# Kernel tuning notes

Measured on AMD Instinct MI355X. Metric: run time of the kernel, lower is better.

The kernel has to match this reference:

```python
import math
import jax, jax.numpy as jnp
import numpy as np

MAX_CH = 21
D_CONV = 1024
LAT_DIM = 5
N_HEADS = 2            # TST_encoder hard-codes n_heads=2 (not PatchTSTEncoder's n_heads=8)
D_FF = 256
L_RAW = 38400
CONV_SPECS = [(512, 10, 5, 1), (512, 3, 2, 1), (512, 3, 2, 1), (1024, 3, 2, 1)]  # (dim,k,stride,dilation)
T_FRAMES = 959         # ((((38400-10)//5+1 -3)//2+1 -3)//2+1 -3)//2+1
T_TOTAL = MAX_CH * T_FRAMES  # 20139
L_LAT = MAX_CH * LAT_DIM     # 105


def sinusoid_table(n, d):
    pos = jnp.arange(n, dtype=jnp.float32)[:, None]
    div = jnp.exp(jnp.arange(0, d, 2, dtype=jnp.float32) * (-math.log(10000.0) / d))
    pe = jnp.zeros((n, d), jnp.float32)
    pe = pe.at[:, 0::2].set(jnp.sin(pos * div))
    pe = pe.at[:, 1::2].set(jnp.cos(pos * div))
    return pe


def setup_inputs() -> dict:
    key = jax.random.key(0)
    ks = jax.random.split(key, 16)
    x = jax.random.normal(ks[0], (1, MAX_CH, L_RAW), dtype=jnp.float32)
    # per-channel validity mask: first 17 of 21 channels valid, broadcast over frames
    ch_valid = jnp.arange(MAX_CH) < 17
    ch_mask = jnp.repeat(ch_valid, T_FRAMES)[None, None, :]  # (1,1,T_TOTAL) bool

    conv_params = {}
    in_c = 1
    for i, (dim, k, s, dil) in enumerate(CONV_SPECS):
        std = 1.0 / math.sqrt(in_c * k)
        conv_params[f"conv_w{i+1}"] = jax.random.normal(ks[1 + i], (dim, in_c, k), jnp.float32) * std
        conv_params[f"conv_b{i+1}"] = jnp.zeros((dim,), jnp.float32)
        in_c = dim

    ch_emb = sinusoid_table(MAX_CH, D_CONV)  # trainable channel embedding, sinusoidal init
    latent_q = jax.random.normal(ks[6], (L_LAT, D_CONV), jnp.float32) * math.sqrt(2.0 / (L_LAT + D_CONV))
    std_d = 1.0 / math.sqrt(D_CONV)
    wk_w = jax.random.normal(ks[7], (D_CONV, D_CONV), jnp.float32) * std_d
    wk_b = jnp.zeros((D_CONV,), jnp.float32)
    wv_w = jax.random.normal(ks[8], (D_CONV, D_CONV), jnp.float32) * std_d
    wv_b = jnp.zeros((D_CONV,), jnp.float32)
    ff_w1 = jax.random.normal(ks[9], (D_FF, D_CONV), jnp.float32) * std_d   # Linear(d_conv->d_ff), no bias
    ff_w2 = jax.random.normal(ks[10], (D_CONV, D_FF), jnp.float32) * (1.0 / math.sqrt(D_FF))
    return dict(x=x,
                conv_w1=conv_params["conv_w1"], conv_b1=conv_params["conv_b1"],
                conv_w2=conv_params["conv_w2"], conv_b2=conv_params["conv_b2"],
                conv_w3=conv_params["conv_w3"], conv_b3=conv_params["conv_b3"],
                conv_w4=conv_params["conv_w4"], conv_b4=conv_params["conv_b4"],
                ch_emb=ch_emb, latent_q=latent_q,
                wk_w=wk_w, wk_b=wk_b, wv_w=wv_w, wv_b=wv_b,
                ff_w1=ff_w1, ff_w2=ff_w2, ch_mask=ch_mask)


def _conv1d(x, w, b, stride, dilation):
    # x: (N, C_in, L), w: (C_out, C_in, K)
    y = jax.lax.conv_general_dilated(x, w, window_strides=(stride,), padding='VALID',
                                     rhs_dilation=(dilation,),
                                     dimension_numbers=('NCH', 'OIH', 'NCH'))
    return y + b[None, :, None]


def reference(x, conv_w1, conv_b1, conv_w2, conv_b2, conv_w3, conv_b3, conv_w4, conv_b4,
              ch_emb, latent_q, wk_w, wk_b, wv_w, wv_b, ff_w1, ff_w2, ch_mask):
    b, c_in, L = x.shape
    # --- ConvFeatureExtraction: per-channel conv stack (dropout is identity at eval) ---
    h = x.reshape(b * c_in, 1, L)
    weights = [(conv_w1, conv_b1), (conv_w2, conv_b2), (conv_w3, conv_b3), (conv_w4, conv_b4)]
    for (w, bi), (_, k, s, dil) in zip(weights, CONV_SPECS):
        h = jax.nn.gelu(_conv1d(h, w, bi, s, dil), approximate=False)
    t = h.shape[-1]
    x_conv = h.reshape(b, c_in, D_CONV, t).transpose(0, 1, 3, 2)  # (b, c_in, t, d_conv)

    # --- DataEmbedding: temporal sinusoid (buffer) + channel embedding (param) ---
    pe = sinusoid_table(t, D_CONV)                                # (t, d_conv)
    x_pos = x_conv + pe[None, None] + ch_emb[None, :, None, :]
    u = x_pos.reshape(b, c_in * t, D_CONV)                        # (1, T, d_conv)

    # --- perceiver_resampler (pre_norm=False: no LayerNorms applied) ---
    T = u.shape[1]
    d_h = D_CONV // N_HEADS
    lq = latent_q.reshape(1, N_HEADS, L_LAT, d_h)                 # exact torch .view semantics
    kproj = (u @ wk_w.T + wk_b).reshape(b, T, N_HEADS, d_h)
    vproj = (u @ wv_w.T + wv_b).reshape(b, T, N_HEADS, d_h)
    k = kproj.transpose(0, 2, 3, 1)                               # (b, H, d, T)
    v = vproj.transpose(0, 2, 1, 3)                               # (b, H, T, d)
    scale = N_HEADS ** (-0.5)                                     # note: heads, not d_k
    scores = jnp.einsum('bhld,bhdt->bhlt', lq, k) * scale         # (b, H, L_lat, T)
    mask = ch_mask[:, None, :, :]                                 # (b,1,1,T) -> broadcast
    scores = jnp.where(mask, scores, -1000000000.0)
    attn = jax.nn.softmax(scores, axis=-1)
    attn = jnp.where(mask, attn, 0.0)
    o = jnp.einsum('bhlt,bhtd->bhld', attn, v)                    # (b, H, L_lat, d)
    o = o.transpose(0, 2, 1, 3).reshape(b, L_LAT, D_CONV)

    # --- GELU FFN (bias=False) + residual ---
    ffn = jax.nn.gelu(o @ ff_w1.T, approximate=False) @ ff_w2.T
    return o + ffn
```

## Files before the change

kernel.cpp:

```cpp
#include <hip/hip_runtime.h>
#include <math.h>


#define NCH 17
#define LRAW 38400
#define LC1 7679
#define LC2 3839
#define LC3 1919
#define LC4 959
#define XA1 3840
#define XA2 1920
#define XA3 960
#define DC 1024
#define TVALID (NCH * LC4)
#define TPAD 16320
#define LLAT 105
#define DH 512
#define ASTR 40
#define GMAX 9
#define ESTR 132

typedef unsigned short u16;
typedef __attribute__((ext_vector_type(8))) short bf16x8;
typedef __attribute__((ext_vector_type(4))) float f32x4;

__device__ __forceinline__ float bf2f(u16 s) {
    union { unsigned int u; float f; } cv; cv.u = ((unsigned int)s) << 16; return cv.f;
}
__device__ __forceinline__ u16 f2bf(float f) {
    union { float f; unsigned int u; } cv; cv.f = f;
    unsigned int u = cv.u;
    u += 0x7FFFu + ((u >> 16) & 1u);
    return (u16)(u >> 16);
}
__device__ __forceinline__ float gelu_exact(float x) {
    return 0.5f * x * (1.0f + erff(x * 0.70710678118654752f));
}
__device__ __forceinline__ float gelu_fast(float x) {
    float u = 0.7978845608f * x * (1.0f + 0.044715f * x * x);
    u = fminf(fmaxf(u, -9.0f), 9.0f);
    float e = __expf(2.0f * u);
    return 0.5f * x * (1.0f + (e - 1.0f) / (e + 1.0f));
}

__device__ __forceinline__ void gload16(const u16* g, u16* l) {
    __builtin_amdgcn_global_load_lds(
        (const __attribute__((address_space(1))) void*)g,
        (__attribute__((address_space(3))) void*)l, 16, 0, 0);
}

__device__ __forceinline__ int xcd_logical(int d, int N) {
    int q = N >> 3, r = N & 7, x = d & 7, j = d >> 3;
    return (x < r ? x * (q + 1) : r * (q + 1) + (x - r) * q) + j;
}

#define STAGE_TILE(lds, src, row0, ld, k0)                                          \
    {                                                                               \
        int m_ = tid >> 2, c_ = tid & 3;                                            \
        gload16(&(src)[(size_t)((row0) + m_) * (ld) + (k0) + ((c_ ^ ((m_ >> 1) & 3)) << 3)], \
                &(lds)[m_ * 32 + c_ * 8]);                                          \
        int m2_ = m_ + 64;                                                          \
        gload16(&(src)[(size_t)((row0) + m2_) * (ld) + (k0) + ((c_ ^ ((m2_ >> 1) & 3)) << 3)], \
                &(lds)[m2_ * 32 + c_ * 8]);                                         \
    }

#define FRAG(lds, R) \
    (*reinterpret_cast<const bf16x8*>(&(lds)[(R) * 32 + ((l4 ^ (((R) >> 1) & 3)) << 3)]))

__global__ void __launch_bounds__(256) cvt_kernel(
        const float* __restrict__ in, u16* __restrict__ out, int n) {
    int i = blockIdx.x * 256 + threadIdx.x;
    if (i < n) out[i] = f2bf(in[i]);
}

__global__ void __launch_bounds__(256) wsplit_kernel(
        const float* __restrict__ w, u16* __restrict__ out, int dout) {
    int idx = blockIdx.x * 256 + threadIdx.x;
    if (idx >= dout * 1536) return;
    int d = idx / 1536, k = idx - d * 1536;
    int ci = k / 3, jj = k - ci * 3;
    out[((size_t)jj * dout + d) * 512 + ci] = f2bf(w[idx]);
}

__global__ void __launch_bounds__(256) lqcvt_kernel(
        const float* __restrict__ lq, u16* __restrict__ lqbf) {
    int idx = blockIdx.x * 256 + threadIdx.x;
    if (idx >= 2 * 128 * 512) return;
    int h = idx >> 16, rem = idx & 65535;
    int m = rem >> 9, k = rem & 511;
    lqbf[idx] = (m < LLAT) ? f2bf(lq[(size_t)h * LLAT * DH + m * DH + k]) : (u16)0;
}

__global__ void __launch_bounds__(256) pe_kernel(float* __restrict__ pe) {
    int idx = blockIdx.x * 256 + threadIdx.x;
    if (idx >= LC4 * 512) return;
    int t = idx / 512, i = idx - (idx / 512) * 512;
    float f = expf((-2.0f * (float)i) * (9.210340371976184f / 1024.0f));
    float ang = (float)t * f;
    pe[t * DC + 2 * i]     = sinf(ang);
    pe[t * DC + 2 * i + 1] = cosf(ang);
}

__global__ void __launch_bounds__(256) conv1_kernel(
        const float* __restrict__ x, const float* __restrict__ w1,
        const float* __restrict__ b1, u16* __restrict__ out, int g0) {
    __shared__ float xs[64 * 5 + 5];
    int cg = blockIdx.y;
    int c  = g0 + cg;
    int t0 = blockIdx.x * 64;
    int nseg = min(64, LC1 - t0);
    int xlen = nseg * 5 + 5;
    const float* xrow = x + (size_t)c * LRAW + t0 * 5;
    int tid = threadIdx.x;
    if (tid < xlen) xs[tid] = xrow[tid];
    if (tid + 256 < xlen) xs[tid + 256] = xrow[tid + 256];
    int d0 = tid * 2;
    float wr0[10], wr1[10];
    #pragma unroll
    for (int j = 0; j < 10; ++j) {
        wr0[j] = w1[d0 * 10 + j];
        wr1[j] = w1[(d0 + 1) * 10 + j];
    }
    float bb0 = b1[d0], bb1 = b1[d0 + 1];
    __syncthreads();
    u16* outc = out + (size_t)cg * 2 * XA1 * 512;
    for (int tt = 0; tt < nseg; ++tt) {
        float a0 = bb0, a1 = bb1;
        #pragma unroll
        for (int j = 0; j < 10; ++j) {
            float xv = xs[tt * 5 + j];
            a0 += wr0[j] * xv;
            a1 += wr1[j] * xv;
        }
        int t = t0 + tt;
        ushort2 wv;
        wv.x = f2bf(gelu_fast(a0));
        wv.y = f2bf(gelu_fast(a1));
        *reinterpret_cast<ushort2*>(
            &outc[((size_t)(t & 1) * XA1 + (t >> 1)) * 512 + d0]) = wv;
    }
}

template <int DOUT, int XIN, int XOUT, int LOUT, int EPI, int NNT, int NMT>
__global__ void __launch_bounds__(256, 4) conv_mfma(
        const u16* __restrict__ in, const u16* __restrict__ wsplit,
        const float* __restrict__ bias, u16* __restrict__ out,
        const float* __restrict__ pe, const float* __restrict__ chemb,
        int g0) {
    __shared__ __align__(16) u16 SH[128 * ESTR];
    u16* const Asb[2] = {SH, SH + 4096};
    u16* const Bsb[2] = {SH + 8192, SH + 12288};
    int L = xcd_logical(blockIdx.x, gridDim.x);
    int mt = L % NMT;
    int rest = L / NMT;
    int nt = rest % NNT;
    int cg = rest / NNT;
    int m0 = mt * 128, n0 = nt * 128;
    int tid = threadIdx.x, lane = tid & 63, wave = tid >> 6;
    int wm = (wave >> 1) * 64, wn = (wave & 1) * 64;
    int l15 = lane & 15, l4 = lane >> 4;
    const u16* bufc = in + (size_t)cg * 2 * XIN * 512;
    const u16* wjp[3] = {wsplit, wsplit + (size_t)DOUT * 512,
                         wsplit + 2 * (size_t)DOUT * 512};
    const u16* bjp[3] = {bufc, bufc + (size_t)XIN * 512, bufc + 512};
    f32x4 acc[4][4] = {};

#define C_STAGE(s, buf)                                   \
    {                                                     \
        int jj_ = (s) >> 4, kk_ = ((s) & 15) << 5;        \
        STAGE_TILE(Asb[buf], wjp[jj_], m0, 512, kk_);     \
        STAGE_TILE(Bsb[buf], bjp[jj_], n0, 512, kk_);     \
    }
#define C_COMPUTE(buf)                                                        \
    {                                                                         \
        bf16x8 af[4], bfr[4];                                                 \
        _Pragma("unroll")                                                     \
        for (int mi = 0; mi < 4; ++mi) af[mi]  = FRAG(Asb[buf], wm + mi * 16 + l15); \
        _Pragma("unroll")                                                     \
        for (int ni = 0; ni < 4; ++ni) bfr[ni] = FRAG(Bsb[buf], wn + ni * 16 + l15); \
        _Pragma("unroll")                                                     \
        for (int mi = 0; mi < 4; ++mi)                                        \
            _Pragma("unroll")                                                 \
            for (int ni = 0; ni < 4; ++ni)                                    \
                acc[mi][ni] = __builtin_amdgcn_mfma_f32_16x16x32_bf16(        \
                    af[mi], bfr[ni], acc[mi][ni], 0, 0, 0);                   \
    }

    C_STAGE(0, 0);
    __syncthreads();
    for (int s = 0; s < 48; s += 2) {
        C_STAGE(s + 1, 1);
        C_COMPUTE(0);
        __syncthreads();
        if (s + 2 < 48) C_STAGE(s + 2, 0);
        C_COMPUTE(1);
        __syncthreads();
    }
#undef C_STAGE
#undef C_COMPUTE

    #pragma unroll
    for (int mi = 0; mi < 4; ++mi) {
        int ml = wm + mi * 16 + l4 * 4;
        #pragma unroll
        for (int ni = 0; ni < 4; ++ni) {
            int nl = wn + ni * 16 + l15;
            ushort4 sv;
            sv.x = f2bf(acc[mi][ni][0]); sv.y = f2bf(acc[mi][ni][1]);
            sv.z = f2bf(acc[mi][ni][2]); sv.w = f2bf(acc[mi][ni][3]);
            *reinterpret_cast<ushort4*>(&SH[nl * ESTR + ml]) = sv;
        }
    }
    __syncthreads();
    int row = tid >> 1, half = tid & 1;
    int t = n0 + row;
    if (t < LOUT) {
        const u16* srow = &SH[row * ESTR + half * 64];
        int d0 = m0 + half * 64;
        if (EPI == 0) {
            u16* dst = out + ((size_t)cg * 2 + (t & 1)) * (size_t)XOUT * 512
                           + (size_t)(t >> 1) * 512 + d0;
            #pragma unroll
            for (int q = 0; q < 8; ++q) {
                bf16x8 sv = *reinterpret_cast<const bf16x8*>(&srow[q * 8]);
                bf16x8 ov;
                #pragma unroll
                for (int e = 0; e < 8; ++e)
                    ov[e] = (short)f2bf(gelu_fast(bf2f((u16)sv[e]) + bias[d0 + q * 8 + e]));
                *reinterpret_cast<bf16x8*>(&dst[q * 8]) = ov;
            }
        } else {
            int c = g0 + cg;
            u16* dst = out + ((size_t)c * LC4 + t) * DC + d0;
            const float* per = &pe[(size_t)t * DC + d0];
            const float* chr = &chemb[(size_t)c * DC + d0];
            #pragma unroll
            for (int q = 0; q < 8; ++q) {
                bf16x8 sv = *reinterpret_cast<const bf16x8*>(&srow[q * 8]);
                bf16x8 ov;
                #pragma unroll
                for (int e = 0; e < 8; ++e)
                    ov[e] = (short)f2bf(gelu_fast(bf2f((u16)sv[e]) + bias[d0 + q * 8 + e])
                                        + per[q * 8 + e] + chr[q * 8 + e]);
                *reinterpret_cast<bf16x8*>(&dst[q * 8]) = ov;
            }
        }
    }
}

__global__ void __launch_bounds__(256, 4) projkv_mfma(
        const u16* __restrict__ u, const u16* __restrict__ wkv,
        const float* __restrict__ kb, const float* __restrict__ vb,
        u16* __restrict__ K, u16* __restrict__ Vt) {
    __shared__ __align__(16) u16 SH[128 * ESTR];
    u16* const Asb[2] = {SH, SH + 4096};
    u16* const Bsb[2] = {SH + 8192, SH + 12288};
    int L = xcd_logical(blockIdx.x, gridDim.x);
    int nt = L & 15;
    int mt = L >> 4;
    int m0 = mt * 128, n0 = nt * 128;
    int tid = threadIdx.x, lane = tid & 63, wave = tid >> 6;
    int wm = (wave >> 1) * 64, wn = (wave & 1) * 64;
    int l15 = lane & 15, l4 = lane >> 4;
    f32x4 acc[4][4] = {};

#define P_STAGE(s, buf)                               \
    {                                                 \
        int kk_ = (s) << 5;                           \
        STAGE_TILE(Asb[buf], u,   m0, DC, kk_);       \
        STAGE_TILE(Bsb[buf], wkv, n0, DC, kk_);       \
    }
#define P_COMPUTE(buf)                                                        \
    {                                                                         \
        bf16x8 af[4], bfr[4];                                                 \
        _Pragma("unroll")                                                     \
        for (int mi = 0; mi < 4; ++mi) af[mi]  = FRAG(Asb[buf], wm + mi * 16 + l15); \
        _Pragma("unroll")                                                     \
        for (int ni = 0; ni < 4; ++ni) bfr[ni] = FRAG(Bsb[buf], wn + ni * 16 + l15); \
        _Pragma("unroll")                                                     \
        for (int mi = 0; mi < 4; ++mi)                                        \
            _Pragma("unroll")                                                 \
            for (int ni = 0; ni < 4; ++ni)                                    \
                acc[mi][ni] = __builtin_amdgcn_mfma_f32_16x16x32_bf16(        \
                    af[mi], bfr[ni], acc[mi][ni], 0, 0, 0);                   \
    }

    P_STAGE(0, 0);
    __syncthreads();
    for (int s = 0; s < 32; s += 2) {
        P_STAGE(s + 1, 1);
        P_COMPUTE(0);
        __syncthreads();
        if (s + 2 < 32) P_STAGE(s + 2, 0);
        P_COMPUTE(1);
        __syncthreads();
    }
#undef P_STAGE
#undef P_COMPUTE

    if (n0 < 1024) {
        #pragma unroll
        for (int mi = 0; mi < 4; ++mi) {
            int ml = wm + mi * 16 + l4 * 4;
            #pragma unroll
            for (int ni = 0; ni < 4; ++ni) {
                int nl = wn + ni * 16 + l15;
                #pragma unroll
                for (int r = 0; r < 4; ++r)
                    SH[(ml + r) * ESTR + nl] = f2bf(acc[mi][ni][r]);
            }
        }
        __syncthreads();
        int row = tid >> 1, half = tid & 1;
        int t = m0 + row;
        if (t < TVALID) {
            const u16* srow = &SH[row * ESTR + half * 64];
            int nn = n0 + half * 64;
            u16* dst = K + (size_t)t * DC + nn;
            #pragma unroll
            for (int q = 0; q < 8; ++q) {
                bf16x8 sv = *reinterpret_cast<const bf16x8*>(&srow[q * 8]);
                bf16x8 ov;
                #pragma unroll
                for (int e = 0; e < 8; ++e)
                    ov[e] = (short)f2bf(bf2f((u16)sv[e]) + kb[nn + q * 8 + e]);
                *reinterpret_cast<bf16x8*>(&dst[q * 8]) = ov;
            }
        }
    } else {
        #pragma unroll
        for (int mi = 0; mi < 4; ++mi) {
            int ml = wm + mi * 16 + l4 * 4;
            #pragma unroll
            for (int ni = 0; ni < 4; ++ni) {
                int nl = wn + ni * 16 + l15;
                ushort4 sv;
                sv.x = f2bf(acc[mi][ni][0]); sv.y = f2bf(acc[mi][ni][1]);
                sv.z = f2bf(acc[mi][ni][2]); sv.w = f2bf(acc[mi][ni][3]);
                *reinterpret_cast<ushort4*>(&SH[nl * ESTR + ml]) = sv;
            }
        }
        __syncthreads();
        int row = tid >> 1, half = tid & 1;
        int j = (n0 - 1024) + row;
        int tbase = m0 + half * 64;
        if (tbase < TPAD) {
            float bj = vb[j];
            const u16* srow = &SH[row * ESTR + half * 64];
            u16* dst = Vt + (size_t)j * TPAD + tbase;
            #pragma unroll
            for (int q = 0; q < 8; ++q) {
                bf16x8 sv = *reinterpret_cast<const bf16x8*>(&srow[q * 8]);
                bf16x8 ov;
                #pragma unroll
                for (int e = 0; e < 8; ++e)
                    ov[e] = (short)f2bf(bf2f((u16)sv[e]) + bj);
                *reinterpret_cast<bf16x8*>(&dst[q * 8]) = ov;
            }
        }
    }
}

__global__ void __launch_bounds__(256) scores_mfma(
        const u16* __restrict__ lqbf, const u16* __restrict__ K,
        float* __restrict__ sc) {
    __shared__ __align__(16) u16 As[128 * ASTR];
    __shared__ __align__(16) u16 Bs[128 * ASTR];
    int n0 = blockIdx.x * 128;
    int h  = blockIdx.y;
    int tid = threadIdx.x, lane = tid & 63, wave = tid >> 6;
    int wm = (wave >> 1) * 64, wn = (wave & 1) * 64;
    int l15 = lane & 15, l4 = lane >> 4;
    const u16* lqh = lqbf + (size_t)h * 128 * DH;
    f32x4 acc[4][4] = {};
    for (int k0 = 0; k0 < DH; k0 += 32) {
        #pragma unroll
        for (int p = 0; p < 2; ++p) {
            int f = tid + p * 256;
            int m = f >> 2, kb = f & 3;
            bf16x8 va = *reinterpret_cast<const bf16x8*>(
                &lqh[(size_t)m * DH + k0 + kb * 8]);
            *reinterpret_cast<bf16x8*>(&As[m * ASTR + kb * 8]) = va;
            int n = n0 + m;
            bf16x8 vb;
            if (n < TVALID)
                vb = *reinterpret_cast<const bf16x8*>(
                    &K[(size_t)n * DC + h * DH + k0 + kb * 8]);
            else
                #pragma unroll
                for (int j = 0; j < 8; ++j) vb[j] = 0;
            *reinterpret_cast<bf16x8*>(&Bs[m * ASTR + kb * 8]) = vb;
        }
        __syncthreads();
        bf16x8 af[4], bfr[4];
        #pragma unroll
        for (int mi = 0; mi < 4; ++mi)
            af[mi] = *reinterpret_cast<const bf16x8*>(
                &As[(wm + mi * 16 + l15) * ASTR + l4 * 8]);
        #pragma unroll
        for (int ni = 0; ni < 4; ++ni)
            bfr[ni] = *reinterpret_cast<const bf16x8*>(
                &Bs[(wn + ni * 16 + l15) * ASTR + l4 * 8]);
        #pragma unroll
        for (int mi = 0; mi < 4; ++mi)
            #pragma unroll
            for (int ni = 0; ni < 4; ++ni)
                acc[mi][ni] = __builtin_amdgcn_mfma_f32_16x16x32_bf16(
                    af[mi], bfr[ni], acc[mi][ni], 0, 0, 0);
        __syncthreads();
    }
    #pragma unroll
    for (int mi = 0; mi < 4; ++mi) {
        int mbase = wm + mi * 16 + l4 * 4;
        #pragma unroll
        for (int ni = 0; ni < 4; ++ni) {
            int t = n0 + wn + ni * 16 + l15;
            if (t >= TVALID) continue;
            #pragma unroll
            for (int r = 0; r < 4; ++r) {
                int m = mbase + r;
                if (m < LLAT)
                    sc[((size_t)h * LLAT + m) * TVALID + t] =
                        acc[mi][ni][r] * 0.70710678118654752f;
            }
        }
    }
}

__global__ void __launch_bounds__(256) softmax_bf16(
        const float* __restrict__ sc, u16* __restrict__ attnP) {
    int r = blockIdx.x;
    const float* row = sc + (size_t)r * TVALID;
    u16* orow = attnP + (size_t)r * TPAD;
    __shared__ float red[8];
    int tid = threadIdx.x;
    float m = -1e30f;
    for (int i = tid; i < TVALID; i += 256) m = fmaxf(m, row[i]);
    #pragma unroll
    for (int off = 32; off > 0; off >>= 1) m = fmaxf(m, __shfl_down(m, off, 64));
    if ((tid & 63) == 0) red[tid >> 6] = m;
    __syncthreads();
    m = fmaxf(fmaxf(red[0], red[1]), fmaxf(red[2], red[3]));
    float s = 0.f;
    for (int i = tid; i < TVALID; i += 256) s += expf(row[i] - m);
    #pragma unroll
    for (int off = 32; off > 0; off >>= 1) s += __shfl_down(s, off, 64);
    if ((tid & 63) == 0) red[4 + (tid >> 6)] = s;
    __syncthreads();
    s = red[4] + red[5] + red[6] + red[7];
    float inv = 1.0f / s;
    for (int i = tid; i < TPAD; i += 256)
        orow[i] = (i < TVALID) ? f2bf(expf(row[i] - m) * inv) : (u16)0;
}

__global__ void __launch_bounds__(256) pv_mfma(
        const u16* __restrict__ attnP, const u16* __restrict__ Vt,
        float* __restrict__ o) {
    __shared__ __align__(16) u16 As[128 * ASTR];
    __shared__ __align__(16) u16 Bs[128 * ASTR];
    int n0 = blockIdx.x * 128;
    int kc = blockIdx.y;
    int h  = blockIdx.z;
    int tid = threadIdx.x, lane = tid & 63, wave = tid >> 6;
    int wm = (wave >> 1) * 64, wn = (wave & 1) * 64;
    int l15 = lane & 15, l4 = lane >> 4;
    f32x4 acc[4][4] = {};
    for (int it = 0; it < 15; ++it) {
        int k0 = (kc * 15 + it) * 32;
        #pragma unroll
        for (int p = 0; p < 2; ++p) {
            int f = tid + p * 256;
            int m = f >> 2, kb = f & 3;
            bf16x8 va;
            if (m < LLAT)
                va = *reinterpret_cast<const bf16x8*>(
                    &attnP[((size_t)h * LLAT + m) * TPAD + k0 + kb * 8]);
            else
                #pragma unroll
                for (int j = 0; j < 8; ++j) va[j] = 0;
            *reinterpret_cast<bf16x8*>(&As[m * ASTR + kb * 8]) = va;
            bf16x8 vb = *reinterpret_cast<const bf16x8*>(
                &Vt[((size_t)h * DH + n0 + m) * TPAD + k0 + kb * 8]);
            *reinterpret_cast<bf16x8*>(&Bs[m * ASTR + kb * 8]) = vb;
        }
        __syncthreads();
        bf16x8 af[4], bfr[4];
        #pragma unroll
        for (int mi = 0; mi < 4; ++mi)
            af[mi] = *reinterpret_cast<const bf16x8*>(
                &As[(wm + mi * 16 + l15) * ASTR + l4 * 8]);
        #pragma unroll
        for (int ni = 0; ni < 4; ++ni)
            bfr[ni] = *reinterpret_cast<const bf16x8*>(
                &Bs[(wn + ni * 16 + l15) * ASTR + l4 * 8]);
        #pragma unroll
        for (int mi = 0; mi < 4; ++mi)
            #pragma unroll
            for (int ni = 0; ni < 4; ++ni)
                acc[mi][ni] = __builtin_amdgcn_mfma_f32_16x16x32_bf16(
                    af[mi], bfr[ni], acc[mi][ni], 0, 0, 0);
        __syncthreads();
    }
    #pragma unroll
    for (int mi = 0; mi < 4; ++mi) {
        int mbase = wm + mi * 16 + l4 * 4;
        #pragma unroll
        for (int ni = 0; ni < 4; ++ni) {
            int n = n0 + wn + ni * 16 + l15;
            #pragma unroll
            for (int r = 0; r < 4; ++r) {
                int m = mbase + r;
                if (m < LLAT)
                    atomicAdd(&o[(size_t)m * DC + h * DH + n], acc[mi][ni][r]);
            }
        }
    }
}

__global__ void __launch_bounds__(256) ffn1_kernel(
        const float* __restrict__ o, const float* __restrict__ w1,
        float* __restrict__ h1) {
    __shared__ float os[DC];
    int l = blockIdx.x;
    for (int i = threadIdx.x; i < DC; i += 256) os[i] = o[(size_t)l * DC + i];
    __syncthreads();
    int f = threadIdx.x;
    const float* wr = w1 + (size_t)f * DC;
    float acc = 0.f;
    for (int d = 0; d < DC; ++d) acc += os[d] * wr[d];
    h1[(size_t)l * 256 + f] = gelu_exact(acc);
}

__global__ void __launch_bounds__(256) ffn2_kernel(
        const float* __restrict__ o, const float* __restrict__ h1,
        const float* __restrict__ w2, float* __restrict__ out) {
    __shared__ float hs[256];
    int l = blockIdx.x;
    hs[threadIdx.x] = h1[(size_t)l * 256 + threadIdx.x];
    __syncthreads();
    for (int d = threadIdx.x; d < DC; d += 256) {
        const float* wr = w2 + (size_t)d * 256;
        float acc = 0.f;
        for (int f = 0; f < 256; ++f) acc += hs[f] * wr[f];
        out[(size_t)l * DC + d] = o[(size_t)l * DC + d] + acc;
    }
}

constexpr size_t OFF_PE  = 0;
constexpr size_t OFF_WB2 = 3928064;
constexpr size_t OFF_WB3 = 5500928;
constexpr size_t OFF_WB4 = 7073792;
constexpr size_t OFF_WKV = 10219520;
constexpr size_t OFF_U   = 14413888;
constexpr size_t OFF_SCR1 = 47968320;
constexpr size_t OFF_SCR2 = 118747200;
constexpr size_t OFF_K   = 47968320;
constexpr size_t OFF_VT  = 81522752;
constexpr size_t OFF_SC  = 114946112;
constexpr size_t OFF_AP  = 128640640;
constexpr size_t OFF_LQ  = 135495040;
constexpr size_t OFF_O   = 135757184;
constexpr size_t OFF_H   = 136187264;

extern "C" void kernel_launch(void* const* d_in, const int* in_sizes, int n_in,
                              void* d_out, int out_size, void* d_ws, size_t ws_size,
                              hipStream_t stream) {
    (void)in_sizes; (void)n_in; (void)out_size; (void)ws_size;
    const float* x     = (const float*)d_in[0];
    const float* w1    = (const float*)d_in[1];
    const float* b1    = (const float*)d_in[2];
    const float* w2    = (const float*)d_in[3];
    const float* b2    = (const float*)d_in[4];
    const float* w3    = (const float*)d_in[5];
    const float* b3    = (const float*)d_in[6];
    const float* w4    = (const float*)d_in[7];
    const float* b4    = (const float*)d_in[8];
    const float* chemb = (const float*)d_in[9];
    const float* latq  = (const float*)d_in[10];
    const float* wkw   = (const float*)d_in[11];
    const float* wkb   = (const float*)d_in[12];
    const float* wvw   = (const float*)d_in[13];
    const float* wvb   = (const float*)d_in[14];
    const float* fw1   = (const float*)d_in[15];
    const float* fw2   = (const float*)d_in[16];
    float* out = (float*)d_out;
    char*  ws  = (char*)d_ws;

    float* pe    = (float*)(ws + OFF_PE);
    u16*   w2s   = (u16*)(ws + OFF_WB2);
    u16*   w3s   = (u16*)(ws + OFF_WB3);
    u16*   w4s   = (u16*)(ws + OFF_WB4);
    u16*   wkv   = (u16*)(ws + OFF_WKV);
    u16*   ubuf  = (u16*)(ws + OFF_U);
    u16*   s1    = (u16*)(ws + OFF_SCR1);
    u16*   s2    = (u16*)(ws + OFF_SCR2);
    u16*   Kbuf  = (u16*)(ws + OFF_K);
    u16*   Vt    = (u16*)(ws + OFF_VT);
    float* sc    = (float*)(ws + OFF_SC);
    u16*   attnP = (u16*)(ws + OFF_AP);
    u16*   lqbf  = (u16*)(ws + OFF_LQ);
    float* obuf  = (float*)(ws + OFF_O);
    float* h1    = (float*)(ws + OFF_H);

    wsplit_kernel<<<(512 * 1536 + 255) / 256, 256, 0, stream>>>(w2, w2s, 512);
    wsplit_kernel<<<(512 * 1536 + 255) / 256, 256, 0, stream>>>(w3, w3s, 512);
    wsplit_kernel<<<(1024 * 1536 + 255) / 256, 256, 0, stream>>>(w4, w4s, 1024);
    cvt_kernel<<<(DC * DC + 255) / 256, 256, 0, stream>>>(wkw, wkv, DC * DC);
    cvt_kernel<<<(DC * DC + 255) / 256, 256, 0, stream>>>(wvw, wkv + (size_t)1024 * DC, DC * DC);
    pe_kernel<<<(LC4 * 512 + 255) / 256, 256, 0, stream>>>(pe);

    for (int g0 = 0; g0 < NCH; g0 += GMAX) {
        int G = (NCH - g0 < GMAX) ? (NCH - g0) : GMAX;
        conv1_kernel<<<dim3((LC1 + 63) / 64, G), 256, 0, stream>>>(x, w1, b1, s1, g0);
        conv_mfma<512, XA1, XA2, LC2, 0, 30, 4><<<30 * 4 * G, 256, 0, stream>>>(
            s1, w2s, b2, s2, nullptr, nullptr, g0);
        conv_mfma<512, XA2, XA3, LC3, 0, 15, 4><<<15 * 4 * G, 256, 0, stream>>>(
            s2, w3s, b3, s1, nullptr, nullptr, g0);
        conv_mfma<1024, XA3, 0, LC4, 1, 8, 8><<<8 * 8 * G, 256, 0, stream>>>(
            s1, w4s, b4, ubuf, pe, chemb, g0);
    }

    projkv_mfma<<<16 * 128, 256, 0, stream>>>(ubuf, wkv, wkb, wvb, Kbuf, Vt);

    lqcvt_kernel<<<(2 * 128 * 512 + 255) / 256, 256, 0, stream>>>(latq, lqbf);
    scores_mfma<<<dim3(128, 2), 256, 0, stream>>>(lqbf, Kbuf, sc);
    softmax_bf16<<<210, 256, 0, stream>>>(sc, attnP);
    hipMemsetAsync(obuf, 0, (size_t)LLAT * DC * sizeof(float), stream);
    pv_mfma<<<dim3(4, 34, 2), 256, 0, stream>>>(attnP, Vt, obuf);
    ffn1_kernel<<<LLAT, 256, 0, stream>>>(obuf, fw1, h1);
    ffn2_kernel<<<LLAT, 256, 0, stream>>>(obuf, h1, fw2, out);
}
```

Baseline: 675.0 us.

## Use partial vmcnt waits and raw barriers to overlap staging with MFMA

Replaces the full __syncthreads in the conv and projection GEMM main loops with explicit s_waitcnt vmcnt(4) plus s_barrier. A wave now waits only for the older stage's global-to-LDS loads, and the next stage's loads stay in flight during compute. It also raises wave priority around the MFMA blocks and unrolls the loop. The gain depends on the async loads completing in order under vmcnt accounting, and the partial wait could create hazards if the count assumption is wrong.

After: 718.3 us. 6.4% more time.

```diff
diff --git a/kernel.cpp b/kernel.cpp
--- a/kernel.cpp
+++ b/kernel.cpp
@@ -66,6 +66,11 @@
 
 #define FRAG(lds, R) \
     (*reinterpret_cast<const bf16x8*>(&(lds)[(R) * 32 + ((l4 ^ (((R) >> 1) & 3)) << 3)]))
+
+#define WAITV4() asm volatile("s_waitcnt vmcnt(4)" ::: "memory")
+#define WAITV0() asm volatile("s_waitcnt vmcnt(0)" ::: "memory")
+#define SBAR()   __builtin_amdgcn_s_barrier()
+#define SCHED0() __builtin_amdgcn_sched_barrier(0)
 
 __global__ void __launch_bounds__(256) cvt_kernel(
         const float* __restrict__ in, u16* __restrict__ out, int n) {
@@ -178,23 +183,32 @@
         for (int mi = 0; mi < 4; ++mi) af[mi]  = FRAG(Asb[buf], wm + mi * 16 + l15); \
         _Pragma("unroll")                                                     \
         for (int ni = 0; ni < 4; ++ni) bfr[ni] = FRAG(Bsb[buf], wn + ni * 16 + l15); \
+        __builtin_amdgcn_s_setprio(1);                                        \
         _Pragma("unroll")                                                     \
         for (int mi = 0; mi < 4; ++mi)                                        \
             _Pragma("unroll")                                                 \
             for (int ni = 0; ni < 4; ++ni)                                    \
                 acc[mi][ni] = __builtin_amdgcn_mfma_f32_16x16x32_bf16(        \
                     af[mi], bfr[ni], acc[mi][ni], 0, 0, 0);                   \
+        __builtin_amdgcn_s_setprio(0);                                        \
     }
 
     C_STAGE(0, 0);
-    __syncthreads();
+    #pragma unroll 4
     for (int s = 0; s < 48; s += 2) {
         C_STAGE(s + 1, 1);
+        WAITV4(); SCHED0(); SBAR(); SCHED0();
         C_COMPUTE(0);
-        __syncthreads();
-        if (s + 2 < 48) C_STAGE(s + 2, 0);
+        SBAR();
+        if (s + 2 < 48) {
+            C_STAGE(s + 2, 0);
+            WAITV4();
+        } else {
+            WAITV0();
+        }
+        SCHED0(); SBAR(); SCHED0();
         C_COMPUTE(1);
-        __syncthreads();
+        SBAR();
     }
 #undef C_STAGE
 #undef C_COMPUTE
@@ -277,23 +291,32 @@
         for (int mi = 0; mi < 4; ++mi) af[mi]  = FRAG(Asb[buf], wm + mi * 16 + l15); \
         _Pragma("unroll")                                                     \
         for (int ni = 0; ni < 4; ++ni) bfr[ni] = FRAG(Bsb[buf], wn + ni * 16 + l15); \
+        __builtin_amdgcn_s_setprio(1);                                        \
         _Pragma("unroll")                                                     \
         for (int mi = 0; mi < 4; ++mi)                                        \
             _Pragma("unroll")                                                 \
             for (int ni = 0; ni < 4; ++ni)                                    \
                 acc[mi][ni] = __builtin_amdgcn_mfma_f32_16x16x32_bf16(        \
                     af[mi], bfr[ni], acc[mi][ni], 0, 0, 0);                   \
+        __builtin_amdgcn_s_setprio(0);                                        \
     }
 
     P_STAGE(0, 0);
-    __syncthreads();
+    #pragma unroll 4
     for (int s = 0; s < 32; s += 2) {
         P_STAGE(s + 1, 1);
+        WAITV4(); SCHED0(); SBAR(); SCHED0();
         P_COMPUTE(0);
-        __syncthreads();
-        if (s + 2 < 32) P_STAGE(s + 2, 0);
+        SBAR();
+        if (s + 2 < 32) {
+            P_STAGE(s + 2, 0);
+            WAITV4();
+        } else {
+            WAITV0();
+        }
+        SCHED0(); SBAR(); SCHED0();
         P_COMPUTE(1);
-        __syncthreads();
+        SBAR();
     }
 #undef P_STAGE
 #undef P_COMPUTE
```
